# Kernel tuning notes

Measured on AMD Instinct MI355X. Metric: run time of the kernel, lower is better.

Reference implementation:

```python
import jax, jax.numpy as jnp
import numpy as np
import math

PHI = (1.0 + math.sqrt(5.0)) / 2.0
TWO_PI = 2.0 * math.pi
LUT_SIZE = 4096  # matches get_global_lut(4096, device)

_LUT_SIN = jnp.sin(jnp.arange(LUT_SIZE, dtype=jnp.float32) * (TWO_PI / LUT_SIZE))
_LUT_COS = jnp.cos(jnp.arange(LUT_SIZE, dtype=jnp.float32) * (TWO_PI / LUT_SIZE))


def lut_sin_cos(theta):
    """Linearly-interpolated sin/cos lookup over a 4096-entry table on [0, 2pi)."""
    pos = jnp.mod(theta, TWO_PI) * (LUT_SIZE / TWO_PI)
    i0f = jnp.floor(pos)
    frac = pos - i0f
    i0 = i0f.astype(jnp.int32) % LUT_SIZE
    i1 = (i0 + 1) % LUT_SIZE
    sin_v = _LUT_SIN[i0] * (1.0 - frac) + _LUT_SIN[i1] * frac
    cos_v = _LUT_COS[i0] * (1.0 - frac) + _LUT_COS[i1] * frac
    return sin_v, cos_v


def setup_inputs() -> dict:
    key = jax.random.key(0)
    ks = jax.random.split(key, 6)
    B, D = 8192, 2048
    return {
        "x_real": jax.random.normal(ks[0], (B, D), dtype=jnp.float32),
        "x_imag": jax.random.normal(ks[1], (B, D), dtype=jnp.float32),
        "t": jax.random.uniform(ks[2], (B,), dtype=jnp.float32) * 100.0,
        "w_query": jax.random.normal(ks[3], (D,), dtype=jnp.float32) * 0.02,
        "b_query": jnp.zeros((D,), dtype=jnp.float32),
        "w_osc": jax.random.normal(ks[4], (D,), dtype=jnp.float32) * 0.02,
        "b_osc": jnp.zeros((D,), dtype=jnp.float32),
        "memory_real": jnp.zeros((B, D), dtype=jnp.float32),
        "memory_imag": jnp.zeros((B, D), dtype=jnp.float32),
    }


def reference(x_real, x_imag, t, w_query, b_query, w_osc, b_osc,
              memory_real, memory_imag):
    d_model = x_real.shape[-1]
    scale = math.sqrt(d_model)
    k = 1.0  # default sensitivity

    t_phi = t[:, None] * PHI  # [B, 1]

    # Query phase via LUT
    wl_query = 1.0 + jnp.abs(w_query)
    theta_query = x_real / wl_query + b_query
    sin_q, cos_q = lut_sin_cos(theta_query)  # query_imag, query_real

    # complex_full interference
    interf_real = jnp.sum(cos_q * x_real + sin_q * x_imag, axis=-1)  # [B]
    interf_imag = jnp.sum(cos_q * x_imag - sin_q * x_real, axis=-1)  # [B]
    interference = jnp.sqrt(interf_real ** 2 + interf_imag ** 2)
    interference_norm = jax.nn.sigmoid(interference / scale - 2.0)
    x_inv = 1.0 - interference_norm
    alpha = jnp.exp(-k * x_inv)[:, None]  # [B, 1]

    # Exponential memory blend (memory is detached / constant)
    blended_real = alpha * x_real + (1.0 - alpha) * memory_real
    blended_imag = alpha * x_imag + (1.0 - alpha) * memory_imag

    # Oscillator evolution via second LUT pass
    wl_osc = 1.0 + jnp.abs(w_osc)
    theta_osc_real = blended_real / wl_osc + b_osc + t_phi
    theta_osc_imag = blended_imag / wl_osc + b_osc + t_phi
    sin_or, cos_or = lut_sin_cos(theta_osc_real)
    sin_oi, cos_oi = lut_sin_cos(theta_osc_imag)
    evolved_real = cos_or * cos_oi - sin_or * sin_oi
    evolved_imag = cos_or * sin_oi + sin_or * cos_oi
    return evolved_real, evolved_imag
```

## Files before the change

### kernel.cpp

```cpp
#include <hip/hip_runtime.h>
#include <math.h>


#define PHI_F 1.61803398874989f

__global__ __launch_bounds__(256) void liquid_echo_kernel(
    const float* __restrict__ x_real, const float* __restrict__ x_imag,
    const float* __restrict__ t_arr,
    const float* __restrict__ w_query, const float* __restrict__ b_query,
    const float* __restrict__ w_osc,   const float* __restrict__ b_osc,
    const float* __restrict__ mem_r,   const float* __restrict__ mem_i,
    float* __restrict__ out_r, float* __restrict__ out_i,
    int D, float inv_scale)
{
    const int row = blockIdx.x;
    const int d4  = D >> 2;
    const size_t base4 = (size_t)row * d4;

    const float4* xr4 = (const float4*)x_real + base4;
    const float4* xi4 = (const float4*)x_imag + base4;
    const float4* wq4 = (const float4*)w_query;
    const float4* bq4 = (const float4*)b_query;

    float4 xr[4], xi[4];
    float accR = 0.f, accI = 0.f;

    #pragma unroll
    for (int s = 0; s < 4; ++s) {
        int c = (int)threadIdx.x + (s << 8);
        if (c < d4) {
            xr[s] = xr4[c];
            xi[s] = xi4[c];
            float4 wq = wq4[c];
            float4 bq = bq4[c];
            #pragma unroll
            for (int j = 0; j < 4; ++j) {
                float xrv = (&xr[s].x)[j];
                float xiv = (&xi[s].x)[j];
                float wl  = 1.f + fabsf((&wq.x)[j]);
                float theta = xrv * __builtin_amdgcn_rcpf(wl) + (&bq.x)[j];
                float sq, cq;
                __sincosf(theta, &sq, &cq);
                accR = fmaf(cq, xrv, fmaf(sq, xiv, accR));
                accI = fmaf(cq, xiv, fmaf(-sq, xrv, accI));
            }
        }
    }

    #pragma unroll
    for (int off = 32; off > 0; off >>= 1) {
        accR += __shfl_down(accR, off);
        accI += __shfl_down(accI, off);
    }
    __shared__ float sR[4], sI[4];
    __shared__ float sAlpha;
    const int wave = threadIdx.x >> 6;
    const int lane = threadIdx.x & 63;
    if (lane == 0) { sR[wave] = accR; sI[wave] = accI; }
    __syncthreads();
    if (threadIdx.x == 0) {
        float ir = sR[0] + sR[1] + sR[2] + sR[3];
        float ii = sI[0] + sI[1] + sI[2] + sI[3];
        float interf = sqrtf(fmaf(ir, ir, ii * ii));
        float z = fmaf(interf, inv_scale, -2.0f);
        float sig = 1.f / (1.f + __expf(-z));
        sAlpha = __expf(-(1.f - sig));
    }
    __syncthreads();

    const float alpha = sAlpha;
    const float beta  = 1.f - alpha;
    const float tphi2 = 2.0f * PHI_F * t_arr[row];

    const float4* wo4 = (const float4*)w_osc;
    const float4* bo4 = (const float4*)b_osc;
    const float4* mr4 = (const float4*)mem_r + base4;
    const float4* mi4 = (const float4*)mem_i + base4;
    float4* or4 = (float4*)out_r + base4;
    float4* oi4 = (float4*)out_i + base4;

    #pragma unroll
    for (int s = 0; s < 4; ++s) {
        int c = (int)threadIdx.x + (s << 8);
        if (c < d4) {
            float4 wo = wo4[c];
            float4 bo = bo4[c];
            float4 mr = mr4[c];
            float4 mi = mi4[c];
            float4 oR, oI;
            #pragma unroll
            for (int j = 0; j < 4; ++j) {
                float br = fmaf(alpha, (&xr[s].x)[j], beta * (&mr.x)[j]);
                float bi = fmaf(alpha, (&xi[s].x)[j], beta * (&mi.x)[j]);
                float wl = 1.f + fabsf((&wo.x)[j]);
                float ang = fmaf(br + bi, __builtin_amdgcn_rcpf(wl),
                                 fmaf(2.f, (&bo.x)[j], tphi2));
                float sv, cv;
                __sincosf(ang, &sv, &cv);
                (&oR.x)[j] = cv;
                (&oI.x)[j] = sv;
            }
            or4[c] = oR;
            oi4[c] = oI;
        }
    }
}

extern "C" void kernel_launch(void* const* d_in, const int* in_sizes, int n_in,
                              void* d_out, int out_size, void* d_ws, size_t ws_size,
                              hipStream_t stream) {
    const float* x_real   = (const float*)d_in[0];
    const float* x_imag   = (const float*)d_in[1];
    const float* t_arr    = (const float*)d_in[2];
    const float* w_query  = (const float*)d_in[3];
    const float* b_query  = (const float*)d_in[4];
    const float* w_osc    = (const float*)d_in[5];
    const float* b_osc    = (const float*)d_in[6];
    const float* mem_r    = (const float*)d_in[7];
    const float* mem_i    = (const float*)d_in[8];

    const int B = in_sizes[2];
    const int D = in_sizes[3];

    float* out_r = (float*)d_out;
    float* out_i = out_r + (size_t)B * D;

    const float inv_scale = 1.0f / sqrtf((float)D);

    liquid_echo_kernel<<<B, 256, 0, stream>>>(
        x_real, x_imag, t_arr, w_query, b_query, w_osc, b_osc,
        mem_r, mem_i, out_r, out_i, D, inv_scale);
}
```

Baseline: 322.9 us.

## Map one row per wavefront to drop block-level syncs and shared reduction

Each 64-lane wavefront now owns a whole row, so the interference reduction is done purely with xor shuffles and every lane computes alpha itself, removing both __syncthreads and the shared-memory stage. Each lane keeps eight float4 pairs of x in registers and uses two accumulator pairs for extra ILP. Launch bounds now request higher occupancy, which may pressure registers given the larger per-thread working set.

```diff
diff --git a/kernel.cpp b/kernel.cpp
--- a/kernel.cpp
+++ b/kernel.cpp
@@ -4,73 +4,80 @@
 
 #define PHI_F 1.61803398874989f
 
-__global__ __launch_bounds__(256) void liquid_echo_kernel(
+__global__ __launch_bounds__(256, 4) void liquid_echo_kernel(
     const float* __restrict__ x_real, const float* __restrict__ x_imag,
     const float* __restrict__ t_arr,
     const float* __restrict__ w_query, const float* __restrict__ b_query,
     const float* __restrict__ w_osc,   const float* __restrict__ b_osc,
     const float* __restrict__ mem_r,   const float* __restrict__ mem_i,
     float* __restrict__ out_r, float* __restrict__ out_i,
-    int D, float inv_scale)
+    int D, int B, float inv_scale)
 {
-    const int row = blockIdx.x;
-    const int d4  = D >> 2;
+    const int wave = (int)threadIdx.x >> 6;
+    const int lane = (int)threadIdx.x & 63;
+    const int row  = ((int)blockIdx.x << 2) + wave;
+    if (row >= B) return;
+
+    const int d4 = D >> 2;
     const size_t base4 = (size_t)row * d4;
+
+    const float tphi2 = 2.0f * PHI_F * t_arr[row];
 
     const float4* xr4 = (const float4*)x_real + base4;
     const float4* xi4 = (const float4*)x_imag + base4;
     const float4* wq4 = (const float4*)w_query;
     const float4* bq4 = (const float4*)b_query;
 
-    float4 xr[4], xi[4];
-    float accR = 0.f, accI = 0.f;
+    float4 xr[8], xi[8];
+    #pragma unroll
+    for (int c = 0; c < 8; ++c) {
+        int idx = (c << 6) + lane;
+        if (idx < d4) {
+            xr[c] = xr4[idx];
+            xi[c] = xi4[idx];
+        }
+    }
 
+    float accR0 = 0.f, accI0 = 0.f;
+    float accR1 = 0.f, accI1 = 0.f;
     #pragma unroll
-    for (int s = 0; s < 4; ++s) {
-        int c = (int)threadIdx.x + (s << 8);
-        if (c < d4) {
-            xr[s] = xr4[c];
-            xi[s] = xi4[c];
-            float4 wq = wq4[c];
-            float4 bq = bq4[c];
+    for (int c = 0; c < 8; ++c) {
+        int idx = (c << 6) + lane;
+        if (idx < d4) {
+            float4 wq = wq4[idx];
+            float4 bq = bq4[idx];
             #pragma unroll
             for (int j = 0; j < 4; ++j) {
-                float xrv = (&xr[s].x)[j];
-                float xiv = (&xi[s].x)[j];
+                float xrv = (&xr[c].x)[j];
+                float xiv = (&xi[c].x)[j];
                 float wl  = 1.f + fabsf((&wq.x)[j]);
                 float theta = xrv * __builtin_amdgcn_rcpf(wl) + (&bq.x)[j];
                 float sq, cq;
                 __sincosf(theta, &sq, &cq);
-                accR = fmaf(cq, xrv, fmaf(sq, xiv, accR));
-                accI = fmaf(cq, xiv, fmaf(-sq, xrv, accI));
+                if (c & 1) {
+                    accR1 = fmaf(cq, xrv, fmaf(sq, xiv, accR1));
+                    accI1 = fmaf(cq, xiv, fmaf(-sq, xrv, accI1));
+                } else {
+                    accR0 = fmaf(cq, xrv, fmaf(sq, xiv, accR0));
+                    accI0 = fmaf(cq, xiv, fmaf(-sq, xrv, accI0));
+                }
             }
         }
     }
+    float accR = accR0 + accR1;
+    float accI = accI0 + accI1;
 
     #pragma unroll
     for (int off = 32; off > 0; off >>= 1) {
-        accR += __shfl_down(accR, off);
-        accI += __shfl_down(accI, off);
+        accR += __shfl_xor(accR, off);
+        accI += __shfl_xor(accI, off);
     }
-    __shared__ float sR[4], sI[4];
-    __shared__ float sAlpha;
-    const int wave = threadIdx.x >> 6;
-    const int lane = threadIdx.x & 63;
-    if (lane == 0) { sR[wave] = accR; sI[wave] = accI; }
-    __syncthreads();
-    if (threadIdx.x == 0) {
-        float ir = sR[0] + sR[1] + sR[2] + sR[3];
-        float ii = sI[0] + sI[1] + sI[2] + sI[3];
-        float interf = sqrtf(fmaf(ir, ir, ii * ii));
-        float z = fmaf(interf, inv_scale, -2.0f);
-        float sig = 1.f / (1.f + __expf(-z));
-        sAlpha = __expf(-(1.f - sig));
-    }
-    __syncthreads();
 
-    const float alpha = sAlpha;
-    const float beta  = 1.f - alpha;
-    const float tphi2 = 2.0f * PHI_F * t_arr[row];
+    float interf = sqrtf(fmaf(accR, accR, accI * accI));
+    float z     = fmaf(interf, inv_scale, -2.0f);
+    float sig   = 1.f / (1.f + __expf(-z));
+    float alpha = __expf(sig - 1.f);
+    float beta  = 1.f - alpha;
 
     const float4* wo4 = (const float4*)w_osc;
     const float4* bo4 = (const float4*)b_osc;
@@ -80,18 +87,18 @@
     float4* oi4 = (float4*)out_i + base4;
 
     #pragma unroll
-    for (int s = 0; s < 4; ++s) {
-        int c = (int)threadIdx.x + (s << 8);
-        if (c < d4) {
-            float4 wo = wo4[c];
-            float4 bo = bo4[c];
-            float4 mr = mr4[c];
-            float4 mi = mi4[c];
+    for (int c = 0; c < 8; ++c) {
+        int idx = (c << 6) + lane;
+        if (idx < d4) {
+            float4 wo = wo4[idx];
+            float4 bo = bo4[idx];
+            float4 mr = mr4[idx];
+            float4 mi = mi4[idx];
             float4 oR, oI;
             #pragma unroll
             for (int j = 0; j < 4; ++j) {
-                float br = fmaf(alpha, (&xr[s].x)[j], beta * (&mr.x)[j]);
-                float bi = fmaf(alpha, (&xi[s].x)[j], beta * (&mi.x)[j]);
+                float br = fmaf(alpha, (&xr[c].x)[j], beta * (&mr.x)[j]);
+                float bi = fmaf(alpha, (&xi[c].x)[j], beta * (&mi.x)[j]);
                 float wl = 1.f + fabsf((&wo.x)[j]);
                 float ang = fmaf(br + bi, __builtin_amdgcn_rcpf(wl),
                                  fmaf(2.f, (&bo.x)[j], tphi2));
@@ -100,8 +107,8 @@
                 (&oR.x)[j] = cv;
                 (&oI.x)[j] = sv;
             }
-            or4[c] = oR;
-            oi4[c] = oI;
+            or4[idx] = oR;
+            oi4[idx] = oI;
         }
     }
 }
@@ -127,7 +134,8 @@
 
     const float inv_scale = 1.0f / sqrtf((float)D);
 
-    liquid_echo_kernel<<<B, 256, 0, stream>>>(
+    const int grid = (B + 3) >> 2;
+    liquid_echo_kernel<<<grid, 256, 0, stream>>>(
         x_real, x_imag, t_arr, w_query, b_query, w_osc, b_osc,
-        mem_r, mem_i, out_r, out_i, D, inv_scale);
+        mem_r, mem_i, out_r, out_i, D, B, inv_scale);
 }
```

Measured after the change: 326.2 us. Within noise of the previous version (+1.0%).

## Split fused kernel into per-row alpha reduction and elementwise evolve kernels

Applied to the files above, without the earlier changes.

The single fused kernel is replaced by two launches. The first kernel assigns one wavefront per row to compute the interference reduction and alpha, which removes the block-wide shared-memory reduction and both __syncthreads barriers. The second kernel reads alpha from workspace and performs the oscillator evolution. The cost is a second read of x_real and x_imag from global memory plus an extra kernel launch, traded for dropping the block barrier that stalled every row between its two phases.

```diff
diff --git a/kernel.cpp b/kernel.cpp
--- a/kernel.cpp
+++ b/kernel.cpp
@@ -4,105 +4,122 @@
 
 #define PHI_F 1.61803398874989f
 
-__global__ __launch_bounds__(256) void liquid_echo_kernel(
+__device__ __forceinline__ void k1_step(
+    const float4* __restrict__ xr4, const float4* __restrict__ xi4,
+    const float4* __restrict__ wq4, const float4* __restrict__ bq4,
+    int c, float& aR, float& aI)
+{
+    float4 xr = xr4[c];
+    float4 xi = xi4[c];
+    float4 wq = wq4[c];
+    float4 bq = bq4[c];
+    #pragma unroll
+    for (int j = 0; j < 4; ++j) {
+        float xrv = (&xr.x)[j];
+        float xiv = (&xi.x)[j];
+        float wl  = 1.f + fabsf((&wq.x)[j]);
+        float th  = xrv * __builtin_amdgcn_rcpf(wl) + (&bq.x)[j];
+        float sq, cq;
+        __sincosf(th, &sq, &cq);
+        aR = fmaf(cq, xrv, fmaf(sq, xiv, aR));
+        aI = fmaf(cq, xiv, fmaf(-sq, xrv, aI));
+    }
+}
+
+__global__ __launch_bounds__(256) void alpha_kernel(
     const float* __restrict__ x_real, const float* __restrict__ x_imag,
-    const float* __restrict__ t_arr,
     const float* __restrict__ w_query, const float* __restrict__ b_query,
-    const float* __restrict__ w_osc,   const float* __restrict__ b_osc,
-    const float* __restrict__ mem_r,   const float* __restrict__ mem_i,
-    float* __restrict__ out_r, float* __restrict__ out_i,
-    int D, float inv_scale)
+    float* __restrict__ alpha_out,
+    int d4, int B, float inv_scale)
 {
-    const int row = blockIdx.x;
-    const int d4  = D >> 2;
+    const int wave = (int)threadIdx.x >> 6;
+    const int lane = (int)threadIdx.x & 63;
+    const int row  = ((int)blockIdx.x << 2) + wave;
+    if (row >= B) return;
+
     const size_t base4 = (size_t)row * d4;
-
     const float4* xr4 = (const float4*)x_real + base4;
     const float4* xi4 = (const float4*)x_imag + base4;
     const float4* wq4 = (const float4*)w_query;
     const float4* bq4 = (const float4*)b_query;
 
-    float4 xr[4], xi[4];
-    float accR = 0.f, accI = 0.f;
+    float aR0 = 0.f, aI0 = 0.f;
+    float aR1 = 0.f, aI1 = 0.f;
 
-    #pragma unroll
-    for (int s = 0; s < 4; ++s) {
-        int c = (int)threadIdx.x + (s << 8);
-        if (c < d4) {
-            xr[s] = xr4[c];
-            xi[s] = xi4[c];
-            float4 wq = wq4[c];
-            float4 bq = bq4[c];
-            #pragma unroll
-            for (int j = 0; j < 4; ++j) {
-                float xrv = (&xr[s].x)[j];
-                float xiv = (&xi[s].x)[j];
-                float wl  = 1.f + fabsf((&wq.x)[j]);
-                float theta = xrv * __builtin_amdgcn_rcpf(wl) + (&bq.x)[j];
-                float sq, cq;
-                __sincosf(theta, &sq, &cq);
-                accR = fmaf(cq, xrv, fmaf(sq, xiv, accR));
-                accI = fmaf(cq, xiv, fmaf(-sq, xrv, accI));
-            }
+    if (d4 == 512) {
+        #pragma unroll
+        for (int s = 0; s < 8; ++s) {
+            if (s & 1) k1_step(xr4, xi4, wq4, bq4, (s << 6) + lane, aR1, aI1);
+            else       k1_step(xr4, xi4, wq4, bq4, (s << 6) + lane, aR0, aI0);
         }
+    } else {
+        for (int c = lane; c < d4; c += 64)
+            k1_step(xr4, xi4, wq4, bq4, c, aR0, aI0);
     }
+
+    float accR = aR0 + aR1;
+    float accI = aI0 + aI1;
 
     #pragma unroll
     for (int off = 32; off > 0; off >>= 1) {
-        accR += __shfl_down(accR, off);
-        accI += __shfl_down(accI, off);
+        accR += __shfl_xor(accR, off);
+        accI += __shfl_xor(accI, off);
     }
-    __shared__ float sR[4], sI[4];
-    __shared__ float sAlpha;
-    const int wave = threadIdx.x >> 6;
-    const int lane = threadIdx.x & 63;
-    if (lane == 0) { sR[wave] = accR; sI[wave] = accI; }
-    __syncthreads();
-    if (threadIdx.x == 0) {
-        float ir = sR[0] + sR[1] + sR[2] + sR[3];
-        float ii = sI[0] + sI[1] + sI[2] + sI[3];
-        float interf = sqrtf(fmaf(ir, ir, ii * ii));
-        float z = fmaf(interf, inv_scale, -2.0f);
-        float sig = 1.f / (1.f + __expf(-z));
-        sAlpha = __expf(-(1.f - sig));
+
+    if (lane == 0) {
+        float interf = sqrtf(fmaf(accR, accR, accI * accI));
+        float z      = fmaf(interf, inv_scale, -2.0f);
+        float sig    = 1.f / (1.f + __expf(-z));
+        alpha_out[row] = __expf(sig - 1.f);
     }
-    __syncthreads();
+}
 
-    const float alpha = sAlpha;
+__global__ __launch_bounds__(256) void evolve_kernel(
+    const float* __restrict__ x_real, const float* __restrict__ x_imag,
+    const float* __restrict__ t_arr,
+    const float* __restrict__ w_osc, const float* __restrict__ b_osc,
+    const float* __restrict__ mem_r, const float* __restrict__ mem_i,
+    const float* __restrict__ alpha_in,
+    float* __restrict__ out_r, float* __restrict__ out_i,
+    int d4)
+{
+    const int row = blockIdx.x;
+    const float alpha = alpha_in[row];
     const float beta  = 1.f - alpha;
     const float tphi2 = 2.0f * PHI_F * t_arr[row];
 
+    const size_t base4 = (size_t)row * d4;
+    const float4* xr4 = (const float4*)x_real + base4;
+    const float4* xi4 = (const float4*)x_imag + base4;
+    const float4* mr4 = (const float4*)mem_r + base4;
+    const float4* mi4 = (const float4*)mem_i + base4;
     const float4* wo4 = (const float4*)w_osc;
     const float4* bo4 = (const float4*)b_osc;
-    const float4* mr4 = (const float4*)mem_r + base4;
-    const float4* mi4 = (const float4*)mem_i + base4;
     float4* or4 = (float4*)out_r + base4;
     float4* oi4 = (float4*)out_i + base4;
 
-    #pragma unroll
-    for (int s = 0; s < 4; ++s) {
-        int c = (int)threadIdx.x + (s << 8);
-        if (c < d4) {
-            float4 wo = wo4[c];
-            float4 bo = bo4[c];
-            float4 mr = mr4[c];
-            float4 mi = mi4[c];
-            float4 oR, oI;
-            #pragma unroll
-            for (int j = 0; j < 4; ++j) {
-                float br = fmaf(alpha, (&xr[s].x)[j], beta * (&mr.x)[j]);
-                float bi = fmaf(alpha, (&xi[s].x)[j], beta * (&mi.x)[j]);
-                float wl = 1.f + fabsf((&wo.x)[j]);
-                float ang = fmaf(br + bi, __builtin_amdgcn_rcpf(wl),
-                                 fmaf(2.f, (&bo.x)[j], tphi2));
-                float sv, cv;
-                __sincosf(ang, &sv, &cv);
-                (&oR.x)[j] = cv;
-                (&oI.x)[j] = sv;
-            }
-            or4[c] = oR;
-            oi4[c] = oI;
+    for (int c = (int)threadIdx.x; c < d4; c += 256) {
+        float4 xr = xr4[c];
+        float4 xi = xi4[c];
+        float4 mr = mr4[c];
+        float4 mi = mi4[c];
+        float4 wo = wo4[c];
+        float4 bo = bo4[c];
+        float4 oR, oI;
+        #pragma unroll
+        for (int j = 0; j < 4; ++j) {
+            float br = fmaf(alpha, (&xr.x)[j], beta * (&mr.x)[j]);
+            float bi = fmaf(alpha, (&xi.x)[j], beta * (&mi.x)[j]);
+            float wl = 1.f + fabsf((&wo.x)[j]);
+            float ang = fmaf(br + bi, __builtin_amdgcn_rcpf(wl),
+                             fmaf(2.f, (&bo.x)[j], tphi2));
+            float sv, cv;
+            __sincosf(ang, &sv, &cv);
+            (&oR.x)[j] = cv;
+            (&oI.x)[j] = sv;
         }
+        or4[c] = oR;
+        oi4[c] = oI;
     }
 }
 
@@ -121,13 +138,19 @@
 
     const int B = in_sizes[2];
     const int D = in_sizes[3];
+    const int d4 = D >> 2;
 
     float* out_r = (float*)d_out;
     float* out_i = out_r + (size_t)B * D;
+    float* alpha_ws = (float*)d_ws;
 
     const float inv_scale = 1.0f / sqrtf((float)D);
 
-    liquid_echo_kernel<<<B, 256, 0, stream>>>(
-        x_real, x_imag, t_arr, w_query, b_query, w_osc, b_osc,
-        mem_r, mem_i, out_r, out_i, D, inv_scale);
+    const int grid1 = (B + 3) >> 2;
+    alpha_kernel<<<grid1, 256, 0, stream>>>(
+        x_real, x_imag, w_query, b_query, alpha_ws, d4, B, inv_scale);
+
+    evolve_kernel<<<B, 256, 0, stream>>>(
+        x_real, x_imag, t_arr, w_osc, b_osc, mem_r, mem_i, alpha_ws,
+        out_r, out_i, d4);
 }
```

Result: slower. 338.4 us (+4.8%).
